# Kernel optimization log

Hardware: AMD Instinct MI355X
Metric: run time of the kernel (lower is better)

## Reference

```python
import jax, jax.numpy as jnp
import numpy as np

N_NODES = 100000
N_EDGES = 1600000
D = 128
L = 3
BN_EPS = 1e-5


def setup_inputs() -> dict:
    key = jax.random.key(0)
    ks = jax.random.split(key, 6)
    x = jax.random.normal(ks[0], (N_NODES, D), dtype=jnp.float32)
    edge_index = jax.random.randint(ks[1], (2, N_EDGES), 0, N_NODES, dtype=jnp.int64)
    Wl = jax.random.normal(ks[2], (L, D, D), dtype=jnp.float32) / np.sqrt(D)
    bl = jax.random.normal(ks[3], (L, D), dtype=jnp.float32) * 0.01
    Wr = jax.random.normal(ks[4], (L, D, D), dtype=jnp.float32) / np.sqrt(D)
    gamma = jnp.ones((L, D), dtype=jnp.float32)
    beta = jnp.zeros((L, D), dtype=jnp.float32)
    return {"x": x, "edge_index": edge_index, "Wl": Wl, "bl": bl,
            "Wr": Wr, "gamma": gamma, "beta": beta}


def _sage_layer(x, src, dst, inv_deg, Wl_i, bl_i, Wr_i, gamma_i, beta_i):
    # mean aggregation over incoming edges: scatter-add messages then divide by degree
    agg_sum = jax.ops.segment_sum(x[src], dst, num_segments=N_NODES)  # [N, D]
    agg = agg_sum * inv_deg[:, None]
    # SAGEConv: lin_l(agg) (with bias) + lin_r(x) (no bias)
    h = jnp.einsum('nd,hd->nh', agg, Wl_i) + bl_i + jnp.einsum('nd,hd->nh', x, Wr_i)
    # BatchNorm1d (training-mode batch stats, biased variance)
    mean = jnp.mean(h, axis=0)
    var = jnp.mean(jnp.square(h - mean), axis=0)
    h = (h - mean) * jax.lax.rsqrt(var + BN_EPS) * gamma_i + beta_i
    return jax.nn.relu(h)  # dropout is identity in eval mode


def reference(x, edge_index, Wl, bl, Wr, gamma, beta):
    src, dst = edge_index[0], edge_index[1]
    deg = jax.ops.segment_sum(jnp.ones((N_EDGES,), jnp.float32), dst,
                              num_segments=N_NODES)
    inv_deg = 1.0 / jnp.maximum(deg, 1.0)
    for i in range(L):
        h = _sage_layer(x, src, dst, inv_deg, Wl[i], bl[i], Wr[i], gamma[i], beta[i])
        if 0 < i < L - 1:  # middle layers get a scaled residual (shapes match)
            x = x + 0.5 * h
        else:
            x = h
    return x
```

## Files before the change

kernel.cpp:

```cpp
#include <hip/hip_runtime.h>

#define N_NODES 100000
#define N_EDGES 1600000
#define D 128
#define BN_EPS 1e-5f
#define N_BLK ((N_NODES + 255) / 256)
#define N_GB ((N_NODES + 63) / 64)
#define NPART 8
#define FILL_BLOCKS 2048
#define NODES_PER_PART (N_NODES / NPART)

typedef short bf16x8 __attribute__((ext_vector_type(8)));
typedef float f32x4 __attribute__((ext_vector_type(4)));

__device__ inline unsigned short f32_to_bf16_rne(float f) {
    unsigned u = __builtin_bit_cast(unsigned, f);
    u += 0x7fffu + ((u >> 16) & 1u);
    return (unsigned short)(u >> 16);
}
__device__ inline float bf16lo_to_f32(unsigned v) { return __builtin_bit_cast(float, v << 16); }
__device__ inline float bf16hi_to_f32(unsigned v) { return __builtin_bit_cast(float, v & 0xffff0000u); }

__device__ inline void gload_lds16(const void* g, void* l) {
    __builtin_amdgcn_global_load_lds((const __attribute__((address_space(1))) unsigned*)g,
                                     (__attribute__((address_space(3))) unsigned*)l, 16, 0, 0);
}


__global__ __launch_bounds__(256) void k_deg(const int* __restrict__ dst, int* __restrict__ degi) {
    const int part = blockIdx.x & (NPART - 1);
    const int lo = part * NODES_PER_PART;
    const int hi = lo + NODES_PER_PART;
    const int stride = (FILL_BLOCKS / NPART) * 256;
    for (int e = (blockIdx.x >> 3) * 256 + threadIdx.x; e < N_EDGES; e += stride) {
        int d = __builtin_nontemporal_load(dst + e);
        if (d >= lo && d < hi) atomicAdd(&degi[d], 1);
    }
}

__global__ __launch_bounds__(256) void k_blocksum(const int* __restrict__ degi, int* __restrict__ bsum) {
    __shared__ int sm[256];
    int t = threadIdx.x;
    int i = blockIdx.x * 256 + t;
    sm[t] = (i < N_NODES) ? degi[i] : 0;
    __syncthreads();
    for (int off = 128; off > 0; off >>= 1) {
        if (t < off) sm[t] += sm[t + off];
        __syncthreads();
    }
    if (t == 0) bsum[blockIdx.x] = sm[0];
}

__global__ __launch_bounds__(512) void k_scan_bsum(const int* __restrict__ bsum, int* __restrict__ boff) {
    __shared__ int sm[512];
    int t = threadIdx.x;
    int v = (t < N_BLK) ? bsum[t] : 0;
    sm[t] = v;
    __syncthreads();
    for (int off = 1; off < 512; off <<= 1) {
        int u = (t >= off) ? sm[t - off] : 0;
        __syncthreads();
        sm[t] += u;
        __syncthreads();
    }
    if (t < N_BLK) boff[t] = sm[t] - v;
}

__global__ __launch_bounds__(256) void k_rowptr(const int* __restrict__ degi, const int* __restrict__ boff,
                                                int* __restrict__ rowptr, float* __restrict__ inv_deg) {
    __shared__ int sm[256];
    int t = threadIdx.x;
    int i = blockIdx.x * 256 + t;
    int v = (i < N_NODES) ? degi[i] : 0;
    sm[t] = v;
    __syncthreads();
    for (int off = 1; off < 256; off <<= 1) {
        int u = (t >= off) ? sm[t - off] : 0;
        __syncthreads();
        sm[t] += u;
        __syncthreads();
    }
    if (i < N_NODES) {
        int incl = sm[t] + boff[blockIdx.x];
        rowptr[i] = incl - v;
        inv_deg[i] = 1.0f / fmaxf((float)v, 1.0f);
        if (i == N_NODES - 1) rowptr[N_NODES] = incl;
    }
}

__global__ __launch_bounds__(256) void k_fill(const int* __restrict__ src, const int* __restrict__ dst,
                                              const int* __restrict__ rowptr, int* __restrict__ cursor,
                                              int* __restrict__ colidx) {
    const int part = blockIdx.x & (NPART - 1);
    const int lo = part * NODES_PER_PART;
    const int hi = lo + NODES_PER_PART;
    const int stride = (FILL_BLOCKS / NPART) * 256;
    for (int e = (blockIdx.x >> 3) * 256 + threadIdx.x; e < N_EDGES; e += stride) {
        int d = __builtin_nontemporal_load(dst + e);
        if (d >= lo && d < hi) {
            int s = __builtin_nontemporal_load(src + e);
            int pos = atomicAdd(&cursor[d], 1);
            colidx[rowptr[d] + pos] = s;
        }
    }
}


__global__ __launch_bounds__(256) void k_xconv(const float* __restrict__ src, unsigned short* __restrict__ hi) {
    int idx = blockIdx.x * 256 + threadIdx.x;
    if (idx >= N_NODES * 32) return;
    float4 v = ((const float4*)src)[idx];
    uint2 p;
    p.x = (unsigned)f32_to_bf16_rne(v.x) | ((unsigned)f32_to_bf16_rne(v.y) << 16);
    p.y = (unsigned)f32_to_bf16_rne(v.z) | ((unsigned)f32_to_bf16_rne(v.w) << 16);
    ((uint2*)hi)[idx] = p;
}

__global__ __launch_bounds__(256) void k_wconv(const float* __restrict__ src, unsigned short* __restrict__ hi,
                                               unsigned short* __restrict__ lo, int n) {
    int i = blockIdx.x * 256 + threadIdx.x;
    if (i >= n) return;
    float w = src[i];
    unsigned short h = f32_to_bf16_rne(w);
    float rem = w - bf16lo_to_f32((unsigned)h);
    hi[i] = h;
    lo[i] = f32_to_bf16_rne(rem);
}


__global__ __launch_bounds__(256) void k_agg(const unsigned short* __restrict__ xhi,
                                             const int* __restrict__ rowptr, const int* __restrict__ colidx,
                                             const float* __restrict__ inv_deg,
                                             unsigned short* __restrict__ agghi) {
    const int wid = threadIdx.x >> 6;
    const int l = threadIdx.x & 63;
    const int n = blockIdx.x * 4 + wid;
    if (n >= N_NODES) return;
    const int b = rowptr[n], e = rowptr[n + 1];
    const int c8 = l & 15;
    const int g = l >> 4;
    const size_t coff = (size_t)c8 * 16;

    float acc[8];
#pragma unroll
    for (int k = 0; k < 8; k++) acc[k] = 0.f;

    int i = b;
    while (i < e) {
        int chunk = e - i; if (chunk > 64) chunk = 64;
        int myE = __builtin_nontemporal_load(colidx + i + (l < chunk ? l : chunk - 1));
        int j = 0;
        for (; j + 8 <= chunk; j += 8) {
            int s0 = __shfl(myE, j + g);
            int s1 = __shfl(myE, j + 4 + g);
            uint4 v0 = *(const uint4*)((const char*)xhi + (size_t)s0 * 256 + coff);
            uint4 v1 = *(const uint4*)((const char*)xhi + (size_t)s1 * 256 + coff);
            acc[0] += bf16lo_to_f32(v0.x); acc[1] += bf16hi_to_f32(v0.x);
            acc[2] += bf16lo_to_f32(v0.y); acc[3] += bf16hi_to_f32(v0.y);
            acc[4] += bf16lo_to_f32(v0.z); acc[5] += bf16hi_to_f32(v0.z);
            acc[6] += bf16lo_to_f32(v0.w); acc[7] += bf16hi_to_f32(v0.w);
            acc[0] += bf16lo_to_f32(v1.x); acc[1] += bf16hi_to_f32(v1.x);
            acc[2] += bf16lo_to_f32(v1.y); acc[3] += bf16hi_to_f32(v1.y);
            acc[4] += bf16lo_to_f32(v1.z); acc[5] += bf16hi_to_f32(v1.z);
            acc[6] += bf16lo_to_f32(v1.w); acc[7] += bf16hi_to_f32(v1.w);
        }
        for (; j + 4 <= chunk; j += 4) {
            int s0 = __shfl(myE, j + g);
            uint4 v0 = *(const uint4*)((const char*)xhi + (size_t)s0 * 256 + coff);
            acc[0] += bf16lo_to_f32(v0.x); acc[1] += bf16hi_to_f32(v0.x);
            acc[2] += bf16lo_to_f32(v0.y); acc[3] += bf16hi_to_f32(v0.y);
            acc[4] += bf16lo_to_f32(v0.z); acc[5] += bf16hi_to_f32(v0.z);
            acc[6] += bf16lo_to_f32(v0.w); acc[7] += bf16hi_to_f32(v0.w);
        }
        if (j < chunk) {
            int idx = j + g;
            int s0 = __shfl(myE, idx < chunk ? idx : chunk - 1);
            if (idx < chunk) {
                uint4 v0 = *(const uint4*)((const char*)xhi + (size_t)s0 * 256 + coff);
                acc[0] += bf16lo_to_f32(v0.x); acc[1] += bf16hi_to_f32(v0.x);
                acc[2] += bf16lo_to_f32(v0.y); acc[3] += bf16hi_to_f32(v0.y);
                acc[4] += bf16lo_to_f32(v0.z); acc[5] += bf16hi_to_f32(v0.z);
                acc[6] += bf16lo_to_f32(v0.w); acc[7] += bf16hi_to_f32(v0.w);
            }
        }
        i += chunk;
    }
#pragma unroll
    for (int k = 0; k < 8; k++) {
        acc[k] += __shfl_xor(acc[k], 16);
        acc[k] += __shfl_xor(acc[k], 32);
    }
    if (g == 0) {
        float idg = inv_deg[n];
        uint4 p;
        p.x = (unsigned)f32_to_bf16_rne(acc[0] * idg) | ((unsigned)f32_to_bf16_rne(acc[1] * idg) << 16);
        p.y = (unsigned)f32_to_bf16_rne(acc[2] * idg) | ((unsigned)f32_to_bf16_rne(acc[3] * idg) << 16);
        p.z = (unsigned)f32_to_bf16_rne(acc[4] * idg) | ((unsigned)f32_to_bf16_rne(acc[5] * idg) << 16);
        p.w = (unsigned)f32_to_bf16_rne(acc[6] * idg) | ((unsigned)f32_to_bf16_rne(acc[7] * idg) << 16);
        *(uint4*)((char*)agghi + (size_t)n * 256 + coff) = p;
    }
}

__global__ __launch_bounds__(256, 2) void k_gemm(
    const unsigned short* __restrict__ agg_hi, const unsigned short* __restrict__ x_hi,
    const unsigned short* __restrict__ wl_hi, const unsigned short* __restrict__ wl_lo,
    const unsigned short* __restrict__ wr_hi, const unsigned short* __restrict__ wr_lo,
    const float* __restrict__ bl, unsigned short* __restrict__ h, float* __restrict__ partial) {
    __shared__ char lds[32768];
    const int t = threadIdx.x;
    const int w = t >> 6;
    const int l = t & 63;
    const int lr = l & 15;
    const int lg = l >> 4;
    const int base = blockIdx.x * 64;
    const int j0 = w * 32;

    {
#pragma unroll
        for (int i = 0; i < 8; i++) {
            int c = w * 8 + i;
            int ci = c & 15;
            int m = ci >> 2, kk = ci & 3;
            int n = base + m * 16 + lr;
            if (n > N_NODES - 1) n = N_NODES - 1;
            size_t goff = (size_t)n * 256 + kk * 64 + lg * 16;
            const char* srcp = ((c & 16) ? (const char*)x_hi : (const char*)agg_hi) + goff;
            gload_lds16(srcp, lds + c * 1024);
        }
    }

    f32x4 acc[4][2];
#pragma unroll
    for (int m = 0; m < 4; m++)
#pragma unroll
        for (int f = 0; f < 2; f++) acc[m][f] = (f32x4){0.f, 0.f, 0.f, 0.f};

#pragma unroll
    for (int seg = 0; seg < 2; seg++) {
        const unsigned short* WH = seg ? wr_hi : wl_hi;
        const unsigned short* WLo = seg ? wr_lo : wl_lo;
        bf16x8 wh[4][2], wlo[4][2];
#pragma unroll
        for (int kk = 0; kk < 4; kk++)
#pragma unroll
            for (int f = 0; f < 2; f++) {
                size_t wo = (size_t)(j0 + f * 16 + lr) * D + kk * 32 + lg * 8;
                wh[kk][f] = *(const bf16x8*)(WH + wo);
                wlo[kk][f] = *(const bf16x8*)(WLo + wo);
            }
        asm volatile("" :: "v"(wh[0][0]), "v"(wh[0][1]), "v"(wh[1][0]), "v"(wh[1][1]),
                           "v"(wh[2][0]), "v"(wh[2][1]), "v"(wh[3][0]), "v"(wh[3][1]));
        asm volatile("" :: "v"(wlo[0][0]), "v"(wlo[0][1]), "v"(wlo[1][0]), "v"(wlo[1][1]),
                           "v"(wlo[2][0]), "v"(wlo[2][1]), "v"(wlo[3][0]), "v"(wlo[3][1]));
        if (seg == 0) __syncthreads();
        const int tb = seg * 16384;
#pragma unroll
        for (int kk = 0; kk < 4; kk++) {
            bf16x8 a[4];
#pragma unroll
            for (int m = 0; m < 4; m++)
                a[m] = *(const bf16x8*)(lds + tb + (m * 4 + kk) * 1024 + l * 16);
#pragma unroll
            for (int f = 0; f < 2; f++)
#pragma unroll
                for (int m = 0; m < 4; m++) {
                    acc[m][f] = __builtin_amdgcn_mfma_f32_16x16x32_bf16(a[m], wh[kk][f], acc[m][f], 0, 0, 0);
                    acc[m][f] = __builtin_amdgcn_mfma_f32_16x16x32_bf16(a[m], wlo[kk][f], acc[m][f], 0, 0, 0);
                }
        }
    }

    float s1[2] = {0.f, 0.f}, s2[2] = {0.f, 0.f};
#pragma unroll
    for (int f = 0; f < 2; f++) {
        const int col = j0 + f * 16 + lr;
        const float bias = bl[col];
#pragma unroll
        for (int m = 0; m < 4; m++) {
#pragma unroll
            for (int r = 0; r < 4; r++) {
                int n = base + m * 16 + lg * 4 + r;
                if (n < N_NODES) {
                    float v = acc[m][f][r] + bias;
                    h[(size_t)n * D + col] = f32_to_bf16_rne(v);
                    s1[f] += v;
                    s2[f] += v * v;
                }
            }
        }
    }
#pragma unroll
    for (int f = 0; f < 2; f++) {
        s1[f] += __shfl_xor(s1[f], 16);
        s1[f] += __shfl_xor(s1[f], 32);
        s2[f] += __shfl_xor(s2[f], 16);
        s2[f] += __shfl_xor(s2[f], 32);
    }
    if (l < 16) {
        float* pp = partial + (size_t)blockIdx.x * 256;
        pp[j0 + l] = s1[0];
        pp[j0 + 16 + l] = s1[1];
        pp[128 + j0 + l] = s2[0];
        pp[128 + j0 + 16 + l] = s2[1];
    }
}

__global__ __launch_bounds__(256) void k_bnred(const float* __restrict__ partial, float* __restrict__ bn32) {
    int t = threadIdx.x;
    float s = 0.f;
    for (int b = blockIdx.x; b < N_GB; b += 32)
        s += partial[(size_t)b * 256 + t];
    bn32[blockIdx.x * 256 + t] = s;
}

__global__ __launch_bounds__(256) void k_apply(const unsigned short* __restrict__ h,
                                               const float* __restrict__ bn32,
                                               const float* __restrict__ gamma, const float* __restrict__ beta,
                                               const unsigned short* __restrict__ xres_hi,
                                               unsigned short* __restrict__ out_hi,
                                               float* __restrict__ out_f32, int mode) {
    __shared__ float sa[128], sc[128];
    int t = threadIdx.x;
    if (t < 128) {
        float m1 = 0.f, m2 = 0.f;
#pragma unroll 8
        for (int i = 0; i < 32; i++) {
            m1 += bn32[i * 256 + t];
            m2 += bn32[i * 256 + 128 + t];
        }
        float mean = m1 * (1.0f / N_NODES);
        float var = m2 * (1.0f / N_NODES) - mean * mean;
        float inv = rsqrtf(var + BN_EPS);
        float av = gamma[t] * inv;
        sa[t] = av;
        sc[t] = beta[t] - mean * av;
    }
    __syncthreads();
    int idx = blockIdx.x * 256 + t;
    if (idx >= N_NODES * 32) return;
    int c0 = (idx & 31) * 4;
    uint2 hv = ((const uint2*)h)[idx];
    float r0 = fmaxf(fmaf(bf16lo_to_f32(hv.x), sa[c0], sc[c0]), 0.f);
    float r1 = fmaxf(fmaf(bf16hi_to_f32(hv.x), sa[c0 + 1], sc[c0 + 1]), 0.f);
    float r2 = fmaxf(fmaf(bf16lo_to_f32(hv.y), sa[c0 + 2], sc[c0 + 2]), 0.f);
    float r3 = fmaxf(fmaf(bf16hi_to_f32(hv.y), sa[c0 + 3], sc[c0 + 3]), 0.f);
    if (mode == 1) {
        uint2 xv = ((const uint2*)xres_hi)[idx];
        r0 = fmaf(0.5f, r0, bf16lo_to_f32(xv.x));
        r1 = fmaf(0.5f, r1, bf16hi_to_f32(xv.x));
        r2 = fmaf(0.5f, r2, bf16lo_to_f32(xv.y));
        r3 = fmaf(0.5f, r3, bf16hi_to_f32(xv.y));
    }
    if (mode == 2) {
        ((float4*)out_f32)[idx] = make_float4(r0, r1, r2, r3);
    } else {
        uint2 p;
        p.x = (unsigned)f32_to_bf16_rne(r0) | ((unsigned)f32_to_bf16_rne(r1) << 16);
        p.y = (unsigned)f32_to_bf16_rne(r2) | ((unsigned)f32_to_bf16_rne(r3) << 16);
        ((uint2*)out_hi)[idx] = p;
    }
}


extern "C" void kernel_launch(void* const* d_in, const int* in_sizes, int n_in,
                              void* d_out, int out_size, void* d_ws, size_t ws_size,
                              hipStream_t stream) {
    const float* x_in = (const float*)d_in[0];
    const int* ei = (const int*)d_in[1];
    const float* Wl = (const float*)d_in[2];
    const float* bl = (const float*)d_in[3];
    const float* Wr = (const float*)d_in[4];
    const float* gamma = (const float*)d_in[5];
    const float* beta = (const float*)d_in[6];
    float* out = (float*)d_out;

    char* ws = (char*)d_ws;
    unsigned short* xhiA = (unsigned short*)ws; ws += (size_t)N_NODES * D * 2;
    unsigned short* xhiB = (unsigned short*)ws; ws += (size_t)N_NODES * D * 2;
    unsigned short* agghi = (unsigned short*)ws; ws += (size_t)N_NODES * D * 2;
    int* rowptr = (int*)ws; ws += (size_t)(N_NODES + 1) * 4;
    int* degi = (int*)ws; ws += (size_t)N_NODES * 4;
    int* cursor = (int*)ws; ws += (size_t)N_NODES * 4;
    int* colidx = (int*)ws; ws += (size_t)N_EDGES * 4;
    float* inv_deg = (float*)ws; ws += (size_t)N_NODES * 4;
    int* bsum = (int*)ws; ws += (size_t)N_BLK * 4;
    int* boff = (int*)ws; ws += (size_t)N_BLK * 4;
    unsigned short* wl_hi = (unsigned short*)ws; ws += (size_t)3 * D * D * 2;
    unsigned short* wl_lo = (unsigned short*)ws; ws += (size_t)3 * D * D * 2;
    unsigned short* wr_hi = (unsigned short*)ws; ws += (size_t)3 * D * D * 2;
    unsigned short* wr_lo = (unsigned short*)ws; ws += (size_t)3 * D * D * 2;
    float* partial = (float*)ws; ws += (size_t)N_GB * 256 * 4;
    float* bn32 = (float*)ws; ws += 32 * 256 * 4;

    const int* src = ei;
    const int* dst = ei + N_EDGES;

    hipMemsetAsync(degi, 0, (size_t)N_NODES * 4, stream);
    hipMemsetAsync(cursor, 0, (size_t)N_NODES * 4, stream);
    k_deg<<<FILL_BLOCKS, 256, 0, stream>>>(dst, degi);
    k_blocksum<<<N_BLK, 256, 0, stream>>>(degi, bsum);
    k_scan_bsum<<<1, 512, 0, stream>>>(bsum, boff);
    k_rowptr<<<N_BLK, 256, 0, stream>>>(degi, boff, rowptr, inv_deg);
    k_fill<<<FILL_BLOCKS, 256, 0, stream>>>(src, dst, rowptr, cursor, colidx);

    k_xconv<<<(N_NODES * 32 + 255) / 256, 256, 0, stream>>>(x_in, xhiA);
    k_wconv<<<(3 * D * D + 255) / 256, 256, 0, stream>>>(Wl, wl_hi, wl_lo, 3 * D * D);
    k_wconv<<<(3 * D * D + 255) / 256, 256, 0, stream>>>(Wr, wr_hi, wr_lo, 3 * D * D);

    unsigned short* xin[3] = { xhiA, xhiB, xhiA };
    unsigned short* xout[3] = { xhiB, xhiA, (unsigned short*)0 };
    int mode[3] = { 0, 1, 2 };

    for (int i = 0; i < 3; i++) {
        k_agg<<<(N_NODES + 3) / 4, 256, 0, stream>>>(xin[i], rowptr, colidx, inv_deg, agghi);
        k_gemm<<<N_GB, 256, 0, stream>>>(agghi, xin[i],
                                         wl_hi + (size_t)i * D * D, wl_lo + (size_t)i * D * D,
                                         wr_hi + (size_t)i * D * D, wr_lo + (size_t)i * D * D,
                                         bl + (size_t)i * D, agghi, partial);
        k_bnred<<<32, 256, 0, stream>>>(partial, bn32);
        k_apply<<<(N_NODES * 32 + 255) / 256, 256, 0, stream>>>(agghi, bn32,
                                                                gamma + (size_t)i * D, beta + (size_t)i * D,
                                                                xin[i], xout[i], out, mode[i]);
    }
}
```

Baseline: 607.2 us.

## Fuse neighbor aggregation into GEMM kernel and merge preprocessing launches

```diff
diff --git a/kernel.cpp b/kernel.cpp
--- a/kernel.cpp
+++ b/kernel.cpp
@@ -27,16 +27,39 @@
 }
 
 
-__global__ __launch_bounds__(256) void k_deg(const int* __restrict__ dst, int* __restrict__ degi) {
-    const int part = blockIdx.x & (NPART - 1);
-    const int lo = part * NODES_PER_PART;
-    const int hi = lo + NODES_PER_PART;
-    const int stride = (FILL_BLOCKS / NPART) * 256;
-    for (int e = (blockIdx.x >> 3) * 256 + threadIdx.x; e < N_EDGES; e += stride) {
-        int d = __builtin_nontemporal_load(dst + e);
-        if (d >= lo && d < hi) atomicAdd(&degi[d], 1);
-    }
-}
+__global__ __launch_bounds__(256) void k_prep(const float* __restrict__ x_in, const int* __restrict__ dst,
+                                              const float* __restrict__ Wl, const float* __restrict__ Wr,
+                                              int* __restrict__ degi, unsigned short* __restrict__ xhi,
+                                              unsigned short* __restrict__ wl_hi, unsigned short* __restrict__ wl_lo,
+                                              unsigned short* __restrict__ wr_hi, unsigned short* __restrict__ wr_lo) {
+    {
+        const int part = blockIdx.x & (NPART - 1);
+        const int lo = part * NODES_PER_PART;
+        const int hi = lo + NODES_PER_PART;
+        const int stride = (FILL_BLOCKS / NPART) * 256;
+        for (int e = (blockIdx.x >> 3) * 256 + threadIdx.x; e < N_EDGES; e += stride) {
+            int d = dst[e];
+            if (d >= lo && d < hi) atomicAdd(&degi[d], 1);
+        }
+    }
+    for (int idx = blockIdx.x * 256 + threadIdx.x; idx < N_NODES * 32; idx += FILL_BLOCKS * 256) {
+        float4 v = ((const float4*)x_in)[idx];
+        uint2 p;
+        p.x = (unsigned)f32_to_bf16_rne(v.x) | ((unsigned)f32_to_bf16_rne(v.y) << 16);
+        p.y = (unsigned)f32_to_bf16_rne(v.z) | ((unsigned)f32_to_bf16_rne(v.w) << 16);
+        ((uint2*)xhi)[idx] = p;
+    }
+    for (int i = blockIdx.x * 256 + threadIdx.x; i < 2 * 3 * D * D; i += FILL_BLOCKS * 256) {
+        const float* srcp = (i < 3 * D * D) ? Wl : Wr;
+        int j = (i < 3 * D * D) ? i : i - 3 * D * D;
+        float w = srcp[j];
+        unsigned short h = f32_to_bf16_rne(w);
+        float rem = w - bf16lo_to_f32((unsigned)h);
+        if (i < 3 * D * D) { wl_hi[j] = h; wl_lo[j] = f32_to_bf16_rne(rem); }
+        else               { wr_hi[j] = h; wr_lo[j] = f32_to_bf16_rne(rem); }
+    }
+}
+
 
 __global__ __launch_bounds__(256) void k_blocksum(const int* __restrict__ degi, int* __restrict__ bsum) {
     __shared__ int sm[256];
@@ -51,37 +74,37 @@
     if (t == 0) bsum[blockIdx.x] = sm[0];
 }
 
-__global__ __launch_bounds__(512) void k_scan_bsum(const int* __restrict__ bsum, int* __restrict__ boff) {
-    __shared__ int sm[512];
-    int t = threadIdx.x;
-    int v = (t < N_BLK) ? bsum[t] : 0;
-    sm[t] = v;
+__global__ __launch_bounds__(512) void k_rowptr(const int* __restrict__ degi, const int* __restrict__ bsum,
+                                                int* __restrict__ rowptr, float* __restrict__ inv_deg) {
+    __shared__ int sb[512];
+    __shared__ int sm[256];
+    const int t = threadIdx.x;
+    int bv = (t < N_BLK) ? bsum[t] : 0;
+    sb[t] = bv;
     __syncthreads();
     for (int off = 1; off < 512; off <<= 1) {
-        int u = (t >= off) ? sm[t - off] : 0;
+        int u = (t >= off) ? sb[t - off] : 0;
         __syncthreads();
-        sm[t] += u;
+        sb[t] += u;
         __syncthreads();
     }
-    if (t < N_BLK) boff[t] = sm[t] - v;
-}
-
-__global__ __launch_bounds__(256) void k_rowptr(const int* __restrict__ degi, const int* __restrict__ boff,
-                                                int* __restrict__ rowptr, float* __restrict__ inv_deg) {
-    __shared__ int sm[256];
-    int t = threadIdx.x;
+    const int boff = (blockIdx.x == 0) ? 0 : sb[blockIdx.x - 1];
     int i = blockIdx.x * 256 + t;
-    int v = (i < N_NODES) ? degi[i] : 0;
-    sm[t] = v;
+    int v = 0;
+    if (t < 256) {
+        v = (i < N_NODES) ? degi[i] : 0;
+        sm[t] = v;
+    }
     __syncthreads();
     for (int off = 1; off < 256; off <<= 1) {
-        int u = (t >= off) ? sm[t - off] : 0;
+        int u = 0;
+        if (t < 256 && t >= off) u = sm[t - off];
         __syncthreads();
-        sm[t] += u;
+        if (t < 256) sm[t] += u;
         __syncthreads();
     }
-    if (i < N_NODES) {
-        int incl = sm[t] + boff[blockIdx.x];
+    if (t < 256 && i < N_NODES) {
+        int incl = sm[t] + boff;
         rowptr[i] = incl - v;
         inv_deg[i] = 1.0f / fmaxf((float)v, 1.0f);
         if (i == N_NODES - 1) rowptr[N_NODES] = incl;
@@ -96,113 +119,17 @@
     const int hi = lo + NODES_PER_PART;
     const int stride = (FILL_BLOCKS / NPART) * 256;
     for (int e = (blockIdx.x >> 3) * 256 + threadIdx.x; e < N_EDGES; e += stride) {
-        int d = __builtin_nontemporal_load(dst + e);
+        int d = dst[e];
         if (d >= lo && d < hi) {
-            int s = __builtin_nontemporal_load(src + e);
             int pos = atomicAdd(&cursor[d], 1);
-            colidx[rowptr[d] + pos] = s;
-        }
-    }
-}
-
-
-__global__ __launch_bounds__(256) void k_xconv(const float* __restrict__ src, unsigned short* __restrict__ hi) {
-    int idx = blockIdx.x * 256 + threadIdx.x;
-    if (idx >= N_NODES * 32) return;
-    float4 v = ((const float4*)src)[idx];
-    uint2 p;
-    p.x = (unsigned)f32_to_bf16_rne(v.x) | ((unsigned)f32_to_bf16_rne(v.y) << 16);
-    p.y = (unsigned)f32_to_bf16_rne(v.z) | ((unsigned)f32_to_bf16_rne(v.w) << 16);
-    ((uint2*)hi)[idx] = p;
-}
-
-__global__ __launch_bounds__(256) void k_wconv(const float* __restrict__ src, unsigned short* __restrict__ hi,
-                                               unsigned short* __restrict__ lo, int n) {
-    int i = blockIdx.x * 256 + threadIdx.x;
-    if (i >= n) return;
-    float w = src[i];
-    unsigned short h = f32_to_bf16_rne(w);
-    float rem = w - bf16lo_to_f32((unsigned)h);
-    hi[i] = h;
-    lo[i] = f32_to_bf16_rne(rem);
-}
-
-
-__global__ __launch_bounds__(256) void k_agg(const unsigned short* __restrict__ xhi,
-                                             const int* __restrict__ rowptr, const int* __restrict__ colidx,
-                                             const float* __restrict__ inv_deg,
-                                             unsigned short* __restrict__ agghi) {
-    const int wid = threadIdx.x >> 6;
-    const int l = threadIdx.x & 63;
-    const int n = blockIdx.x * 4 + wid;
-    if (n >= N_NODES) return;
-    const int b = rowptr[n], e = rowptr[n + 1];
-    const int c8 = l & 15;
-    const int g = l >> 4;
-    const size_t coff = (size_t)c8 * 16;
-
-    float acc[8];
-#pragma unroll
-    for (int k = 0; k < 8; k++) acc[k] = 0.f;
-
-    int i = b;
-    while (i < e) {
-        int chunk = e - i; if (chunk > 64) chunk = 64;
-        int myE = __builtin_nontemporal_load(colidx + i + (l < chunk ? l : chunk - 1));
-        int j = 0;
-        for (; j + 8 <= chunk; j += 8) {
-            int s0 = __shfl(myE, j + g);
-            int s1 = __shfl(myE, j + 4 + g);
-            uint4 v0 = *(const uint4*)((const char*)xhi + (size_t)s0 * 256 + coff);
-            uint4 v1 = *(const uint4*)((const char*)xhi + (size_t)s1 * 256 + coff);
-            acc[0] += bf16lo_to_f32(v0.x); acc[1] += bf16hi_to_f32(v0.x);
-            acc[2] += bf16lo_to_f32(v0.y); acc[3] += bf16hi_to_f32(v0.y);
-            acc[4] += bf16lo_to_f32(v0.z); acc[5] += bf16hi_to_f32(v0.z);
-            acc[6] += bf16lo_to_f32(v0.w); acc[7] += bf16hi_to_f32(v0.w);
-            acc[0] += bf16lo_to_f32(v1.x); acc[1] += bf16hi_to_f32(v1.x);
-            acc[2] += bf16lo_to_f32(v1.y); acc[3] += bf16hi_to_f32(v1.y);
-            acc[4] += bf16lo_to_f32(v1.z); acc[5] += bf16hi_to_f32(v1.z);
-            acc[6] += bf16lo_to_f32(v1.w); acc[7] += bf16hi_to_f32(v1.w);
-        }
-        for (; j + 4 <= chunk; j += 4) {
-            int s0 = __shfl(myE, j + g);
-            uint4 v0 = *(const uint4*)((const char*)xhi + (size_t)s0 * 256 + coff);
-            acc[0] += bf16lo_to_f32(v0.x); acc[1] += bf16hi_to_f32(v0.x);
-            acc[2] += bf16lo_to_f32(v0.y); acc[3] += bf16hi_to_f32(v0.y);
-            acc[4] += bf16lo_to_f32(v0.z); acc[5] += bf16hi_to_f32(v0.z);
-            acc[6] += bf16lo_to_f32(v0.w); acc[7] += bf16hi_to_f32(v0.w);
-        }
-        if (j < chunk) {
-            int idx = j + g;
-            int s0 = __shfl(myE, idx < chunk ? idx : chunk - 1);
-            if (idx < chunk) {
-                uint4 v0 = *(const uint4*)((const char*)xhi + (size_t)s0 * 256 + coff);
-                acc[0] += bf16lo_to_f32(v0.x); acc[1] += bf16hi_to_f32(v0.x);
-                acc[2] += bf16lo_to_f32(v0.y); acc[3] += bf16hi_to_f32(v0.y);
-                acc[4] += bf16lo_to_f32(v0.z); acc[5] += bf16hi_to_f32(v0.z);
-                acc[6] += bf16lo_to_f32(v0.w); acc[7] += bf16hi_to_f32(v0.w);
-            }
-        }
-        i += chunk;
-    }
-#pragma unroll
-    for (int k = 0; k < 8; k++) {
-        acc[k] += __shfl_xor(acc[k], 16);
-        acc[k] += __shfl_xor(acc[k], 32);
-    }
-    if (g == 0) {
-        float idg = inv_deg[n];
-        uint4 p;
-        p.x = (unsigned)f32_to_bf16_rne(acc[0] * idg) | ((unsigned)f32_to_bf16_rne(acc[1] * idg) << 16);
-        p.y = (unsigned)f32_to_bf16_rne(acc[2] * idg) | ((unsigned)f32_to_bf16_rne(acc[3] * idg) << 16);
-        p.z = (unsigned)f32_to_bf16_rne(acc[4] * idg) | ((unsigned)f32_to_bf16_rne(acc[5] * idg) << 16);
-        p.w = (unsigned)f32_to_bf16_rne(acc[6] * idg) | ((unsigned)f32_to_bf16_rne(acc[7] * idg) << 16);
-        *(uint4*)((char*)agghi + (size_t)n * 256 + coff) = p;
-    }
-}
-
-__global__ __launch_bounds__(256, 2) void k_gemm(
-    const unsigned short* __restrict__ agg_hi, const unsigned short* __restrict__ x_hi,
+            colidx[rowptr[d] + pos] = src[e];
+        }
+    }
+}
+
+__global__ __launch_bounds__(256, 2) void k_aggemm(
+    const unsigned short* __restrict__ x_hi,
+    const int* __restrict__ rowptr, const int* __restrict__ colidx, const float* __restrict__ inv_deg,
     const unsigned short* __restrict__ wl_hi, const unsigned short* __restrict__ wl_lo,
     const unsigned short* __restrict__ wr_hi, const unsigned short* __restrict__ wr_lo,
     const float* __restrict__ bl, unsigned short* __restrict__ h, float* __restrict__ partial) {
@@ -217,15 +144,83 @@
 
     {
 #pragma unroll
-        for (int i = 0; i < 8; i++) {
-            int c = w * 8 + i;
-            int ci = c & 15;
-            int m = ci >> 2, kk = ci & 3;
+        for (int i = 0; i < 4; i++) {
+            int c = w * 4 + i;
+            int m = c >> 2, kk = c & 3;
             int n = base + m * 16 + lr;
             if (n > N_NODES - 1) n = N_NODES - 1;
             size_t goff = (size_t)n * 256 + kk * 64 + lg * 16;
-            const char* srcp = ((c & 16) ? (const char*)x_hi : (const char*)agg_hi) + goff;
-            gload_lds16(srcp, lds + c * 1024);
+            gload_lds16((const char*)x_hi + goff, lds + 16384 + c * 1024);
+        }
+    }
+
+    {
+        const int c8 = l & 15;
+        const int g = l >> 4;
+        const size_t coff = (size_t)c8 * 16;
+        for (int i = 0; i < 16; i++) {
+            const int n = base + w * 16 + i;
+            float acc[8];
+#pragma unroll
+            for (int k = 0; k < 8; k++) acc[k] = 0.f;
+            if (n < N_NODES) {
+                const int b = rowptr[n], e = rowptr[n + 1];
+                int p = b;
+                while (p < e) {
+                    int chunk = e - p; if (chunk > 64) chunk = 64;
+                    int myE = colidx[p + (l < chunk ? l : chunk - 1)];
+                    int j = 0;
+                    for (; j + 8 <= chunk; j += 8) {
+                        int s0 = __shfl(myE, j + g);
+                        int s1 = __shfl(myE, j + 4 + g);
+                        uint4 v0 = *(const uint4*)((const char*)x_hi + (size_t)s0 * 256 + coff);
+                        uint4 v1 = *(const uint4*)((const char*)x_hi + (size_t)s1 * 256 + coff);
+                        acc[0] += bf16lo_to_f32(v0.x); acc[1] += bf16hi_to_f32(v0.x);
+                        acc[2] += bf16lo_to_f32(v0.y); acc[3] += bf16hi_to_f32(v0.y);
+                        acc[4] += bf16lo_to_f32(v0.z); acc[5] += bf16hi_to_f32(v0.z);
+                        acc[6] += bf16lo_to_f32(v0.w); acc[7] += bf16hi_to_f32(v0.w);
+                        acc[0] += bf16lo_to_f32(v1.x); acc[1] += bf16hi_to_f32(v1.x);
+                        acc[2] += bf16lo_to_f32(v1.y); acc[3] += bf16hi_to_f32(v1.y);
+                        acc[4] += bf16lo_to_f32(v1.z); acc[5] += bf16hi_to_f32(v1.z);
+                        acc[6] += bf16lo_to_f32(v1.w); acc[7] += bf16hi_to_f32(v1.w);
+                    }
+                    for (; j + 4 <= chunk; j += 4) {
+                        int s0 = __shfl(myE, j + g);
+                        uint4 v0 = *(const uint4*)((const char*)x_hi + (size_t)s0 * 256 + coff);
+                        acc[0] += bf16lo_to_f32(v0.x); acc[1] += bf16hi_to_f32(v0.x);
+                        acc[2] += bf16lo_to_f32(v0.y); acc[3] += bf16hi_to_f32(v0.y);
+                        acc[4] += bf16lo_to_f32(v0.z); acc[5] += bf16hi_to_f32(v0.z);
+                        acc[6] += bf16lo_to_f32(v0.w); acc[7] += bf16hi_to_f32(v0.w);
+                    }
+                    if (j < chunk) {
+                        int idx = j + g;
+                        int s0 = __shfl(myE, idx < chunk ? idx : chunk - 1);
+                        if (idx < chunk) {
+                            uint4 v0 = *(const uint4*)((const char*)x_hi + (size_t)s0 * 256 + coff);
+                            acc[0] += bf16lo_to_f32(v0.x); acc[1] += bf16hi_to_f32(v0.x);
+                            acc[2] += bf16lo_to_f32(v0.y); acc[3] += bf16hi_to_f32(v0.y);
+                            acc[4] += bf16lo_to_f32(v0.z); acc[5] += bf16hi_to_f32(v0.z);
+                            acc[6] += bf16lo_to_f32(v0.w); acc[7] += bf16hi_to_f32(v0.w);
+                        }
+                    }
+                    p += chunk;
+                }
+#pragma unroll
+                for (int k = 0; k < 8; k++) {
+                    acc[k] += __shfl_xor(acc[k], 16);
+                    acc[k] += __shfl_xor(acc[k], 32);
+                }
+            }
+            if (g == 0) {
+                float idg = (n < N_NODES) ? inv_deg[n] : 0.f;
+                uint4 pk;
+                pk.x = (unsigned)f32_to_bf16_rne(acc[0] * idg) | ((unsigned)f32_to_bf16_rne(acc[1] * idg) << 16);
+                pk.y = (unsigned)f32_to_bf16_rne(acc[2] * idg) | ((unsigned)f32_to_bf16_rne(acc[3] * idg) << 16);
+                pk.z = (unsigned)f32_to_bf16_rne(acc[4] * idg) | ((unsigned)f32_to_bf16_rne(acc[5] * idg) << 16);
+                pk.w = (unsigned)f32_to_bf16_rne(acc[6] * idg) | ((unsigned)f32_to_bf16_rne(acc[7] * idg) << 16);
+                int addr = ((w * 4 + (c8 >> 2)) << 10) + ((((c8 & 3) << 4) | i) << 4);
+                *(uint4*)(lds + addr) = pk;
+            }
         }
     }
 
@@ -377,14 +372,13 @@
     char* ws = (char*)d_ws;
     unsigned short* xhiA = (unsigned short*)ws; ws += (size_t)N_NODES * D * 2;
     unsigned short* xhiB = (unsigned short*)ws; ws += (size_t)N_NODES * D * 2;
-    unsigned short* agghi = (unsigned short*)ws; ws += (size_t)N_NODES * D * 2;
+    unsigned short* hbuf = (unsigned short*)ws; ws += (size_t)N_NODES * D * 2;
     int* rowptr = (int*)ws; ws += (size_t)(N_NODES + 1) * 4;
     int* degi = (int*)ws; ws += (size_t)N_NODES * 4;
     int* cursor = (int*)ws; ws += (size_t)N_NODES * 4;
     int* colidx = (int*)ws; ws += (size_t)N_EDGES * 4;
     float* inv_deg = (float*)ws; ws += (size_t)N_NODES * 4;
     int* bsum = (int*)ws; ws += (size_t)N_BLK * 4;
-    int* boff = (int*)ws; ws += (size_t)N_BLK * 4;
     unsigned short* wl_hi = (unsigned short*)ws; ws += (size_t)3 * D * D * 2;
     unsigned short* wl_lo = (unsigned short*)ws; ws += (size_t)3 * D * D * 2;
     unsigned short* wr_hi = (unsigned short*)ws; ws += (size_t)3 * D * D * 2;
@@ -395,30 +389,24 @@
     const int* src = ei;
     const int* dst = ei + N_EDGES;
 
-    hipMemsetAsync(degi, 0, (size_t)N_NODES * 4, stream);
-    hipMemsetAsync(cursor, 0, (size_t)N_NODES * 4, stream);
-    k_deg<<<FILL_BLOCKS, 256, 0, stream>>>(dst, degi);
+    hipMemsetAsync(degi, 0, (size_t)2 * N_NODES * 4, stream);
+    k_prep<<<FILL_BLOCKS, 256, 0, stream>>>(x_in, dst, Wl, Wr, degi, xhiA,
+                                            wl_hi, wl_lo, wr_hi, wr_lo);
     k_blocksum<<<N_BLK, 256, 0, stream>>>(degi, bsum);
-    k_scan_bsum<<<1, 512, 0, stream>>>(bsum, boff);
-    k_rowptr<<<N_BLK, 256, 0, stream>>>(degi, boff, rowptr, inv_deg);
+    k_rowptr<<<N_BLK, 512, 0, stream>>>(degi, bsum, rowptr, inv_deg);
     k_fill<<<FILL_BLOCKS, 256, 0, stream>>>(src, dst, rowptr, cursor, colidx);
-
-    k_xconv<<<(N_NODES * 32 + 255) / 256, 256, 0, stream>>>(x_in, xhiA);
-    k_wconv<<<(3 * D * D + 255) / 256, 256, 0, stream>>>(Wl, wl_hi, wl_lo, 3 * D * D);
-    k_wconv<<<(3 * D * D + 255) / 256, 256, 0, stream>>>(Wr, wr_hi, wr_lo, 3 * D * D);
 
     unsigned short* xin[3] = { xhiA, xhiB, xhiA };
     unsigned short* xout[3] = { xhiB, xhiA, (unsigned short*)0 };
     int mode[3] = { 0, 1, 2 };
 
     for (int i = 0; i < 3; i++) {
-        k_agg<<<(N_NODES + 3) / 4, 256, 0, stream>>>(xin[i], rowptr, colidx, inv_deg, agghi);
-        k_gemm<<<N_GB, 256, 0, stream>>>(agghi, xin[i],
-                                         wl_hi + (size_t)i * D * D, wl_lo + (size_t)i * D * D,
-                                         wr_hi + (size_t)i * D * D, wr_lo + (size_t)i * D * D,
-                                         bl + (size_t)i * D, agghi, partial);
+        k_aggemm<<<N_GB, 256, 0, stream>>>(xin[i], rowptr, colidx, inv_deg,
+                                           wl_hi + (size_t)i * D * D, wl_lo + (size_t)i * D * D,
+                                           wr_hi + (size_t)i * D * D, wr_lo + (size_t)i * D * D,
+                                           bl + (size_t)i * D, hbuf, partial);
         k_bnred<<<32, 256, 0, stream>>>(partial, bn32);
-        k_apply<<<(N_NODES * 32 + 255) / 256, 256, 0, stream>>>(agghi, bn32,
+        k_apply<<<(N_NODES * 32 + 255) / 256, 256, 0, stream>>>(hbuf, bn32,
                                                                 gamma + (size_t)i * D, beta + (size_t)i * D,
                                                                 xin[i], xout[i], out, mode[i]);
     }
```

Result: slower. 644.0 us (+6.1%).
